# Optimization experiments

Measured on AMD Instinct MI355X. Metric: run time of the kernel, lower is better.

The kernel has to match this reference:

```python
import jax, jax.numpy as jnp
import numpy as np

NQ = 200000; K = 4; M = 64; KEY = 64; V = 128; E = 64; B = 512; S = 200

def setup_inputs() -> dict:
    key = jax.random.key(0)
    ks = jax.random.split(key, 16)
    return {
        'q_embed_table': jax.random.normal(ks[0], (NQ + 1, E), jnp.float32) * 0.1,
        'alpha_mean': jax.random.normal(ks[1], (NQ,), jnp.float32) * 0.2,
        'beta_base': jax.random.normal(ks[2], (NQ,), jnp.float32) * 0.5,
        'beta_gaps': jax.random.uniform(ks[3], (NQ, K - 2), jnp.float32) * 0.5 + 0.25,
        'ability_means': jax.random.normal(ks[4], (M, V), jnp.float32) * 0.1,
        'ability_log_vars': jnp.zeros((M, V), jnp.float32),
        'memory_keys': jax.random.normal(ks[5], (M, KEY), jnp.float32),
        'q_to_key_w': jax.random.normal(ks[6], (E, KEY), jnp.float32) / np.sqrt(E),
        'q_to_key_b': jnp.zeros((KEY,), jnp.float32),
        'qa_embed_w': jax.random.normal(ks[7], (2, E), jnp.float32),
        'qa_embed_b': jnp.zeros((E,), jnp.float32),
        'qa_to_ev_w': jax.random.normal(ks[8], (E, V), jnp.float32) / np.sqrt(E),
        'qa_to_ev_b': jnp.zeros((V,), jnp.float32),
        'questions': jax.random.randint(ks[9], (B, S), 0, NQ),
        'responses': jax.random.randint(ks[10], (B, S), 0, K),
    }


def reference(q_embed_table, alpha_mean, beta_base, beta_gaps, ability_means,
              ability_log_vars, memory_keys, q_to_key_w, q_to_key_b,
              qa_embed_w, qa_embed_b, qa_to_ev_w, qa_to_ev_b,
              questions, responses):
    nQ = alpha_mean.shape[0]
    Kc = beta_gaps.shape[1] + 2  # n_categories

    # --- gather question-specific IRT params (irregular gather) ---
    alphas = jnp.exp(alpha_mean[questions])                      # [B,S]
    base = beta_base[questions]                                  # [B,S]
    gaps = jax.nn.softplus(beta_gaps[questions])                 # [B,S,K-2]
    # cumulative thresholds: beta_0 = base, beta_k = beta_{k-1} + gap_{k-1}
    betas = jnp.cumsum(jnp.concatenate([base[..., None], gaps], axis=-1), axis=-1)  # [B,S,K-1]

    # --- attention over memory slots ---
    q_emb = q_embed_table[questions]                             # [B,S,E]
    queries = q_emb @ q_to_key_w + q_to_key_b                    # [B,S,KEY]
    attn = jax.nn.softmax(jnp.einsum('bsk,mk->bsm', queries, memory_keys), axis=-1)  # [B,S,M]

    # --- evidence embedding from (question, response) ---
    qn = questions.astype(jnp.float32) / nQ
    rn = responses.astype(jnp.float32) / (Kc - 1)
    qa = jnp.stack([qn, rn], axis=-1) @ qa_embed_w + qa_embed_b  # [B,S,E]
    evidence = jnp.tanh(qa) @ qa_to_ev_w + qa_to_ev_b            # [B,S,V]

    # --- sequential memory read + per-slot Bayesian scatter update ---
    def step(carry, inp):
        means, log_vars = carry                                  # [M,V] each
        attn_t, ev_t = inp                                       # [B,M], [B,V]
        theta = jnp.mean(attn_t @ means, axis=-1)                # bayesian_read -> [B]
        # precision-weighted update of every slot (evidence_precision = 1)
        w = jnp.mean(attn_t, axis=0)                             # [M] update weights
        ev_mean = jnp.mean(ev_t, axis=0)                         # [V]
        prior_prec = jnp.exp(-log_vars)
        post_prec = prior_prec + w[:, None]
        post_mean = (prior_prec * means + ev_mean[None, :] * w[:, None]) / post_prec
        # torch updates under no_grad -> stop_gradient
        new_means = jax.lax.stop_gradient(post_mean)
        new_lv = jax.lax.stop_gradient(-jnp.log(post_prec))
        return (new_means, new_lv), theta

    (_, _), thetas = jax.lax.scan(
        step, (ability_means, ability_log_vars),
        (attn.transpose(1, 0, 2), evidence.transpose(1, 0, 2)))
    thetas = thetas.T                                            # [B,S]

    # --- GPCM category probabilities ---
    z = alphas[..., None] * (thetas[..., None] - betas)          # [B,S,K-1]
    cum = jnp.concatenate([jnp.zeros_like(z[..., :1]), jnp.cumsum(z, axis=-1)], axis=-1)  # [B,S,K]
    probs = jax.nn.softmax(cum, axis=-1)
    return probs
```

## Files before the change

### kernel.cpp

```cpp
#include <hip/hip_runtime.h>
#include <math.h>

#define M_SLOTS 64
#define E_DIM   64
#define KEY_DIM 64
#define V_DIM   128
#define K_CAT   4
#define S_LEN   200

typedef __attribute__((ext_vector_type(8)))  short short8;
typedef __attribute__((ext_vector_type(16))) float f32x16;

#define OFF_CT     0
#define OFF_BM     2048
#define OFF_WBAR   2112
#define OFF_BBAR   2176
#define OFF_RM0    2240
#define OFF_P0     2304
#define OFF_WSUM   2368
#define OFF_EMSUM  (OFF_WSUM + S_LEN*M_SLOTS)
#define ZERO_CNT   (S_LEN*M_SLOTS + S_LEN)

__device__ __forceinline__ unsigned pk2rne(float lo, float hi) {
    unsigned ul = __float_as_uint(lo); ul += 0x7fffu + ((ul >> 16) & 1u);
    unsigned uh = __float_as_uint(hi); uh += 0x7fffu + ((uh >> 16) & 1u);
    return __builtin_amdgcn_perm(uh, ul, 0x07060302u);
}
__device__ __forceinline__ unsigned short bf16rne(float f) {
    unsigned u = __float_as_uint(f);
    return (unsigned short)((u + 0x7fffu + ((u >> 16) & 1u)) >> 16);
}
__device__ __forceinline__ short8 as_s8(uint4 u) { return __builtin_bit_cast(short8, u); }

__device__ __forceinline__ void gpcm_store(float th, int q,
                                           const float* __restrict__ alpha_mean,
                                           const float* __restrict__ beta_base,
                                           const float* __restrict__ beta_gaps,
                                           float* __restrict__ out, size_t idx) {
    float a  = __expf(alpha_mean[q]);
    float b0 = beta_base[q];
    float2 g = *reinterpret_cast<const float2*>(&beta_gaps[q * (K_CAT - 2)]);
    float g0 = log1pf(__expf(g.x));
    float g1 = log1pf(__expf(g.y));
    float be1 = b0 + g0;
    float be2 = be1 + g1;
    float z0 = a * (th - b0);
    float z1 = a * (th - be1);
    float z2 = a * (th - be2);
    float c1 = z0, c2 = z0 + z1, c3 = z0 + z1 + z2;
    float cm = fmaxf(fmaxf(0.f, c1), fmaxf(c2, c3));
    float e0 = __expf(0.f - cm), e1 = __expf(c1 - cm), e2 = __expf(c2 - cm), e3 = __expf(c3 - cm);
    float si = __fdividef(1.0f, e0 + e1 + e2 + e3);
    float4 o4 = make_float4(e0 * si, e1 * si, e2 * si, e3 * si);
    *reinterpret_cast<float4*>(&out[idx * K_CAT]) = o4;
}

__device__ __forceinline__ void load_qf(const float* __restrict__ qrow, int h, float4 qf[8]) {
    #pragma unroll
    for (int s = 0; s < 4; ++s) {
        const float4* src = (const float4*)(qrow + s * 16 + h * 8);
        qf[2 * s]     = src[0];
        qf[2 * s + 1] = src[1];
    }
}

__device__ __forceinline__ void mfma_logits(
    const float4 qf[8], const unsigned short* __restrict__ ct,
    const float* __restrict__ bm, int h, int p, f32x16 acc[2])
{
    uint4 af[8];
    #pragma unroll
    for (int mt = 0; mt < 2; ++mt)
        #pragma unroll
        for (int s = 0; s < 4; ++s)
            af[mt * 4 + s] = *(const uint4*)(ct + (p + 32 * mt) * E_DIM + s * 16 + h * 8);
    #pragma unroll
    for (int mt = 0; mt < 2; ++mt)
        #pragma unroll
        for (int g = 0; g < 4; ++g) {
            float4 v = *(const float4*)(bm + 8 * g + 4 * h + 32 * mt);
            acc[mt][4 * g + 0] = v.x; acc[mt][4 * g + 1] = v.y;
            acc[mt][4 * g + 2] = v.z; acc[mt][4 * g + 3] = v.w;
        }
    #pragma unroll
    for (int s = 0; s < 4; ++s) {
        uint4 bf;
        bf.x = pk2rne(qf[2 * s].x,     qf[2 * s].y);
        bf.y = pk2rne(qf[2 * s].z,     qf[2 * s].w);
        bf.z = pk2rne(qf[2 * s + 1].x, qf[2 * s + 1].y);
        bf.w = pk2rne(qf[2 * s + 1].z, qf[2 * s + 1].w);
        short8 bfr = as_s8(bf);
        acc[0] = __builtin_amdgcn_mfma_f32_32x32x16_bf16(as_s8(af[s]),     bfr, acc[0], 0, 0, 0);
        acc[1] = __builtin_amdgcn_mfma_f32_32x32x16_bf16(as_s8(af[4 + s]), bfr, acc[1], 0, 0, 0);
    }
}

__global__ __launch_bounds__(256) void k_pre(
    const float* __restrict__ q2k_w, const float* __restrict__ q2k_b,
    const float* __restrict__ mkeys,
    const float* __restrict__ ev_w, const float* __restrict__ ev_b,
    const float* __restrict__ means, const float* __restrict__ logvars,
    float* __restrict__ ws)
{
    const int tid = threadIdx.x;
    if (blockIdx.x != 0) {
        int i = ((int)blockIdx.x - 1) * 1024 + tid * 4;
        if (i + 4 <= ZERO_CNT) {
            *reinterpret_cast<float4*>(ws + OFF_WSUM + i) = make_float4(0.f, 0.f, 0.f, 0.f);
        } else {
            for (int j = i; j < ZERO_CNT; ++j) ws[OFF_WSUM + j] = 0.f;
        }
        return;
    }
    const int wv = tid >> 6, lane = tid & 63;
    const int h = lane >> 5, p = lane & 31;

    {
        const int m0 = (wv & 1) * 32, e0 = (wv >> 1) * 32;
        f32x16 d;
        #pragma unroll
        for (int i = 0; i < 16; ++i) d[i] = 0.f;
        #pragma unroll
        for (int s = 0; s < 4; ++s) {
            const float* ar = mkeys + (m0 + p) * KEY_DIM + s * 16 + h * 8;
            const float* br = q2k_w + (e0 + p) * KEY_DIM + s * 16 + h * 8;
            float4 a0 = *(const float4*)ar, a1 = *(const float4*)(ar + 4);
            float4 b0 = *(const float4*)br, b1 = *(const float4*)(br + 4);
            uint4 au, bu;
            au.x = pk2rne(a0.x, a0.y); au.y = pk2rne(a0.z, a0.w);
            au.z = pk2rne(a1.x, a1.y); au.w = pk2rne(a1.z, a1.w);
            bu.x = pk2rne(b0.x, b0.y); bu.y = pk2rne(b0.z, b0.w);
            bu.z = pk2rne(b1.x, b1.y); bu.w = pk2rne(b1.z, b1.w);
            d = __builtin_amdgcn_mfma_f32_32x32x16_bf16(as_s8(au), as_s8(bu), d, 0, 0, 0);
        }
        unsigned short* ct = (unsigned short*)ws;
        #pragma unroll
        for (int j = 0; j < 16; ++j) {
            int row = (j & 3) + 8 * ((j >> 2) & 3) + 4 * h;
            ct[(m0 + row) * E_DIM + e0 + p] = bf16rne(d[j]);
        }
    }

    if (wv == 0) {
        float s = 0.f;
        const float4* er = (const float4*)(ev_w + (size_t)lane * V_DIM);
        #pragma unroll
        for (int i = 0; i < V_DIM / 4; ++i) {
            float4 v = er[i];
            s += (v.x + v.y) + (v.z + v.w);
        }
        ws[OFF_WBAR + lane] = s * (1.0f / V_DIM);
    } else if (wv == 1) {
        float s = 0.f;
        const float4* mk = (const float4*)(mkeys + lane * KEY_DIM);
        const float4* qb = (const float4*)q2k_b;
        #pragma unroll
        for (int i = 0; i < KEY_DIM / 4; ++i) {
            float4 a = mk[i], c = qb[i];
            s += a.x * c.x + a.y * c.y + a.z * c.z + a.w * c.w;
        }
        ws[OFF_BM + lane] = s;
        float bbv = ev_b[lane] + ev_b[64 + lane];
        #pragma unroll
        for (int o = 32; o; o >>= 1) bbv += __shfl_xor(bbv, o);
        if (!lane) ws[OFF_BBAR] = bbv * (1.0f / V_DIM);
    } else if (wv == 2) {
        float s = 0.f;
        const float4* mr = (const float4*)(means + (size_t)lane * V_DIM);
        #pragma unroll
        for (int i = 0; i < V_DIM / 4; ++i) {
            float4 v = mr[i];
            s += (v.x + v.y) + (v.z + v.w);
        }
        ws[OFF_RM0 + lane] = s * (1.0f / V_DIM);
        ws[OFF_P0 + lane]  = __expf(-logvars[(size_t)lane * V_DIM]);
    }
}

__global__ __launch_bounds__(256, 4) void k_attn(
    const float* __restrict__ qtab, const int* __restrict__ qs, const int* __restrict__ rs,
    const float* __restrict__ ws_ro,
    const float* __restrict__ qa_w, const float* __restrict__ qa_b,
    float* __restrict__ wsum, float* __restrict__ emsum,
    int B, float invNQ)
{
    __shared__ float4 lsEv[64];
    const int tid = threadIdx.x, wv = tid >> 6, lane = tid & 63;
    const int h = lane >> 5, p = lane & 31;
    const int t = blockIdx.x;
    const int b = blockIdx.y * 128 + wv * 32 + p;

    const int q = qs[(size_t)b * S_LEN + t];
    const int r = rs[(size_t)b * S_LEN + t];
    float4 qf[8];
    load_qf(qtab + (size_t)q * E_DIM, h, qf);

    if (tid < 64) lsEv[tid] = make_float4(qa_w[tid], qa_w[E_DIM + tid], qa_b[tid],
                                          ws_ro[OFF_WBAR + tid]);
    const float bb = ws_ro[OFF_BBAR];

    f32x16 acc[2];
    mfma_logits(qf, (const unsigned short*)ws_ro, ws_ro + OFF_BM, h, p, acc);

    float av[32];
    float ssum = 0.f;
    #pragma unroll
    for (int j = 0; j < 16; ++j) { av[j]      = __expf(acc[0][j]); ssum += av[j]; }
    #pragma unroll
    for (int j = 0; j < 16; ++j) { av[16 + j] = __expf(acc[1][j]); ssum += av[16 + j]; }
    ssum += __shfl_xor(ssum, 32);
    const float inv = __fdividef(1.0f, ssum);

    #pragma unroll
    for (int j = 0; j < 32; ++j) av[j] *= inv;
    #pragma unroll
    for (int step = 0; step < 5; ++step) {
        const int sh = 1 << step;
        #pragma unroll
        for (int j = 0; j < (32 >> step) / 2; ++j) {
            float p0 = av[2 * j]     + __shfl_xor(av[2 * j], sh);
            float p1 = av[2 * j + 1] + __shfl_xor(av[2 * j + 1], sh);
            av[j] = (lane & sh) ? p1 : p0;
        }
    }
    {
        const int jj = lane & 31;
        const int m = (jj & 3) + 8 * ((jj >> 2) & 3) + 4 * h + 32 * (jj >> 4);
        atomicAdd(&wsum[t * M_SLOTS + m], av[0]);
    }

    __syncthreads();

    float qn = (float)q * invNQ;
    float rn = (float)r * (1.0f / (K_CAT - 1));
    float evm = 0.f;
    #pragma unroll 8
    for (int e = 0; e < 32; ++e) {
        float4 pv = lsEv[h * 32 + e];
        float qa = fmaf(qn, pv.x, fmaf(rn, pv.y, pv.z));
        float ez = __expf(2.0f * qa);
        evm = fmaf(__fdividef(ez - 1.0f, ez + 1.0f), pv.w, evm);
    }
    evm += __shfl_xor(evm, 32);
    evm += bb;
    #pragma unroll
    for (int o = 16; o; o >>= 1) evm += __shfl_xor(evm, o);
    if (!lane) atomicAdd(&emsum[t], evm);
}

__global__ __launch_bounds__(256, 4) void k_out(
    const float* __restrict__ qtab, const int* __restrict__ qs,
    const float* __restrict__ ws_ro,
    const float* __restrict__ alpha_mean, const float* __restrict__ beta_base,
    const float* __restrict__ beta_gaps, float* __restrict__ out, int B, float invB)
{
    __shared__ float lsW[4][M_SLOTS], lsN[4][M_SLOTS];
    __shared__ float lsRmP[M_SLOTS];
    const int tid = threadIdx.x, wv = tid >> 6, lane = tid & 63;
    const int h = lane >> 5, p = lane & 31;
    const int t = blockIdx.x;
    const int b = blockIdx.y * 128 + wv * 32 + p;

    const int q = qs[(size_t)b * S_LEN + t];
    float4 qf[8];
    load_qf(qtab + (size_t)q * E_DIM, h, qf);

    {
        const float* wsum  = ws_ro + OFF_WSUM;
        const float* emsum = ws_ro + OFF_EMSUM;
        const int seg = (t + 3) >> 2;
        const int s0 = wv * seg, s1 = min(s0 + seg, t);
        float pw0 = 0.f, pn0 = 0.f, pw1 = 0.f, pn1 = 0.f;
        int s = s0;
        for (; s + 2 <= s1; s += 2) {
            float w0 = wsum[s * M_SLOTS + lane];
            float w1 = wsum[(s + 1) * M_SLOTS + lane];
            float e0 = emsum[s], e1 = emsum[s + 1];
            pw0 += w0; pn0 = fmaf(e0, w0, pn0);
            pw1 += w1; pn1 = fmaf(e1, w1, pn1);
        }
        if (s < s1) {
            float w = wsum[s * M_SLOTS + lane];
            pw0 += w; pn0 = fmaf(emsum[s], w, pn0);
        }
        lsW[wv][lane] = pw0 + pw1; lsN[wv][lane] = pn0 + pn1;
    }
    __syncthreads();
    if (tid < 64) {
        const int m = tid;
        float sw = lsW[0][m] + lsW[1][m] + lsW[2][m] + lsW[3][m];
        float sn = lsN[0][m] + lsN[1][m] + lsN[2][m] + lsN[3][m];
        float den = ws_ro[OFF_P0 + m] + sw * invB;
        float num = fmaf(ws_ro[OFF_P0 + m], ws_ro[OFF_RM0 + m], sn * (invB * invB));
        const int idx = ((m >> 2) & 1) * 32 + ((m >> 5) & 1) * 16 + (m & 3) + 4 * ((m >> 3) & 3);
        lsRmP[idx] = num / den;
    }
    __syncthreads();

    f32x16 acc[2];
    mfma_logits(qf, (const unsigned short*)ws_ro, ws_ro + OFF_BM, h, p, acc);

    float ssum = 0.f, th = 0.f;
    const float* rmh = lsRmP + h * 32;
    #pragma unroll
    for (int j = 0; j < 16; ++j) {
        float e = __expf(acc[0][j]);
        ssum += e;
        th = fmaf(e, rmh[j], th);
    }
    #pragma unroll
    for (int j = 0; j < 16; ++j) {
        float e = __expf(acc[1][j]);
        ssum += e;
        th = fmaf(e, rmh[16 + j], th);
    }
    ssum += __shfl_xor(ssum, 32);
    th   += __shfl_xor(th, 32);
    th = __fdividef(th, ssum);

    if (!h) gpcm_store(th, q, alpha_mean, beta_base, beta_gaps, out, (size_t)b * S_LEN + t);
}

extern "C" void kernel_launch(void* const* d_in, const int* in_sizes, int n_in,
                              void* d_out, int out_size, void* d_ws, size_t ws_size,
                              hipStream_t stream) {
    const float* qtab       = (const float*)d_in[0];
    const float* alpha_mean = (const float*)d_in[1];
    const float* beta_base  = (const float*)d_in[2];
    const float* beta_gaps  = (const float*)d_in[3];
    const float* ab_means   = (const float*)d_in[4];
    const float* ab_logvars = (const float*)d_in[5];
    const float* mkeys      = (const float*)d_in[6];
    const float* q2k_w      = (const float*)d_in[7];
    const float* q2k_b      = (const float*)d_in[8];
    const float* qa_w       = (const float*)d_in[9];
    const float* qa_b       = (const float*)d_in[10];
    const float* ev_w       = (const float*)d_in[11];
    const float* ev_b       = (const float*)d_in[12];
    const int*   qs         = (const int*)d_in[13];
    const int*   rs         = (const int*)d_in[14];
    float* out = (float*)d_out;
    float* ws  = (float*)d_ws;

    const int NQ = in_sizes[1];
    const int S  = S_LEN;
    const int B  = in_sizes[13] / S;

    float* wsum  = ws + OFF_WSUM;
    float* emsum = ws + OFF_EMSUM;

    k_pre<<<14, 256, 0, stream>>>(q2k_w, q2k_b, mkeys, ev_w, ev_b,
                                  ab_means, ab_logvars, ws);

    dim3 g(S, B / 128);
    k_attn<<<g, 256, 0, stream>>>(qtab, qs, rs, ws, qa_w, qa_b,
                                  wsum, emsum, B, 1.0f / (float)NQ);

    k_out<<<g, 256, 0, stream>>>(qtab, qs, ws, alpha_mean, beta_base,
                                 beta_gaps, out, B, 1.0f / (float)B);
}
```

Measured before the change: 47.16 us.

## Process two timesteps per block in attention and output kernels

Each block of k_attn and k_out now handles two consecutive timesteps instead of one, and the grid's time dimension is halved. In k_out the prefix sum over earlier steps is computed once for t0, and the t1 value is derived by adding a single step, which avoids a second pass over the prefix. The change also issues more independent gathers per thread for latency hiding and lowers the launch-bounds occupancy hint from 4 to 3. In exchange it raises register pressure and leaves fewer blocks to spread across CUs.

```diff
diff --git a/kernel.cpp b/kernel.cpp
--- a/kernel.cpp
+++ b/kernel.cpp
@@ -95,6 +95,35 @@
     }
 }
 
+__device__ __forceinline__ void softmax_fold_store(
+    const f32x16 acc[2], int lane, int h, int t,
+    float* __restrict__ wsum)
+{
+    float av[32];
+    float ssum = 0.f;
+    #pragma unroll
+    for (int j = 0; j < 16; ++j) { av[j]      = __expf(acc[0][j]); ssum += av[j]; }
+    #pragma unroll
+    for (int j = 0; j < 16; ++j) { av[16 + j] = __expf(acc[1][j]); ssum += av[16 + j]; }
+    ssum += __shfl_xor(ssum, 32);
+    const float inv = __fdividef(1.0f, ssum);
+    #pragma unroll
+    for (int j = 0; j < 32; ++j) av[j] *= inv;
+    #pragma unroll
+    for (int step = 0; step < 5; ++step) {
+        const int sh = 1 << step;
+        #pragma unroll
+        for (int j = 0; j < (32 >> step) / 2; ++j) {
+            float p0 = av[2 * j]     + __shfl_xor(av[2 * j], sh);
+            float p1 = av[2 * j + 1] + __shfl_xor(av[2 * j + 1], sh);
+            av[j] = (lane & sh) ? p1 : p0;
+        }
+    }
+    const int jj = lane & 31;
+    const int m = (jj & 3) + 8 * ((jj >> 2) & 3) + 4 * h + 32 * (jj >> 4);
+    atomicAdd(&wsum[t * M_SLOTS + m], av[0]);
+}
+
 __global__ __launch_bounds__(256) void k_pre(
     const float* __restrict__ q2k_w, const float* __restrict__ q2k_b,
     const float* __restrict__ mkeys,
@@ -177,7 +206,7 @@
     }
 }
 
-__global__ __launch_bounds__(256, 4) void k_attn(
+__global__ __launch_bounds__(256, 3) void k_attn(
     const float* __restrict__ qtab, const int* __restrict__ qs, const int* __restrict__ rs,
     const float* __restrict__ ws_ro,
     const float* __restrict__ qa_w, const float* __restrict__ qa_b,
@@ -187,89 +216,81 @@
     __shared__ float4 lsEv[64];
     const int tid = threadIdx.x, wv = tid >> 6, lane = tid & 63;
     const int h = lane >> 5, p = lane & 31;
-    const int t = blockIdx.x;
+    const int t0 = blockIdx.x * 2, t1 = t0 + 1;
     const int b = blockIdx.y * 128 + wv * 32 + p;
 
-    const int q = qs[(size_t)b * S_LEN + t];
-    const int r = rs[(size_t)b * S_LEN + t];
-    float4 qf[8];
-    load_qf(qtab + (size_t)q * E_DIM, h, qf);
+    const int q0 = qs[(size_t)b * S_LEN + t0];
+    const int r0 = rs[(size_t)b * S_LEN + t0];
+    const int q1 = qs[(size_t)b * S_LEN + t1];
+    const int r1 = rs[(size_t)b * S_LEN + t1];
+    float4 qf0[8], qf1[8];
+    load_qf(qtab + (size_t)q0 * E_DIM, h, qf0);
+    load_qf(qtab + (size_t)q1 * E_DIM, h, qf1);
 
     if (tid < 64) lsEv[tid] = make_float4(qa_w[tid], qa_w[E_DIM + tid], qa_b[tid],
                                           ws_ro[OFF_WBAR + tid]);
     const float bb = ws_ro[OFF_BBAR];
 
-    f32x16 acc[2];
-    mfma_logits(qf, (const unsigned short*)ws_ro, ws_ro + OFF_BM, h, p, acc);
-
-    float av[32];
-    float ssum = 0.f;
-    #pragma unroll
-    for (int j = 0; j < 16; ++j) { av[j]      = __expf(acc[0][j]); ssum += av[j]; }
-    #pragma unroll
-    for (int j = 0; j < 16; ++j) { av[16 + j] = __expf(acc[1][j]); ssum += av[16 + j]; }
-    ssum += __shfl_xor(ssum, 32);
-    const float inv = __fdividef(1.0f, ssum);
-
-    #pragma unroll
-    for (int j = 0; j < 32; ++j) av[j] *= inv;
-    #pragma unroll
-    for (int step = 0; step < 5; ++step) {
-        const int sh = 1 << step;
-        #pragma unroll
-        for (int j = 0; j < (32 >> step) / 2; ++j) {
-            float p0 = av[2 * j]     + __shfl_xor(av[2 * j], sh);
-            float p1 = av[2 * j + 1] + __shfl_xor(av[2 * j + 1], sh);
-            av[j] = (lane & sh) ? p1 : p0;
-        }
-    }
     {
-        const int jj = lane & 31;
-        const int m = (jj & 3) + 8 * ((jj >> 2) & 3) + 4 * h + 32 * (jj >> 4);
-        atomicAdd(&wsum[t * M_SLOTS + m], av[0]);
+        f32x16 acc[2];
+        mfma_logits(qf0, (const unsigned short*)ws_ro, ws_ro + OFF_BM, h, p, acc);
+        softmax_fold_store(acc, lane, h, t0, wsum);
+    }
+    {
+        f32x16 acc[2];
+        mfma_logits(qf1, (const unsigned short*)ws_ro, ws_ro + OFF_BM, h, p, acc);
+        softmax_fold_store(acc, lane, h, t1, wsum);
     }
 
     __syncthreads();
 
-    float qn = (float)q * invNQ;
-    float rn = (float)r * (1.0f / (K_CAT - 1));
-    float evm = 0.f;
+    float ev0 = 0.f, ev1 = 0.f;
+    const float qn0 = (float)q0 * invNQ, rn0 = (float)r0 * (1.0f / (K_CAT - 1));
+    const float qn1 = (float)q1 * invNQ, rn1 = (float)r1 * (1.0f / (K_CAT - 1));
     #pragma unroll 8
     for (int e = 0; e < 32; ++e) {
         float4 pv = lsEv[h * 32 + e];
-        float qa = fmaf(qn, pv.x, fmaf(rn, pv.y, pv.z));
-        float ez = __expf(2.0f * qa);
-        evm = fmaf(__fdividef(ez - 1.0f, ez + 1.0f), pv.w, evm);
-    }
-    evm += __shfl_xor(evm, 32);
-    evm += bb;
-    #pragma unroll
-    for (int o = 16; o; o >>= 1) evm += __shfl_xor(evm, o);
-    if (!lane) atomicAdd(&emsum[t], evm);
-}
-
-__global__ __launch_bounds__(256, 4) void k_out(
+        float qa0 = fmaf(qn0, pv.x, fmaf(rn0, pv.y, pv.z));
+        float qa1 = fmaf(qn1, pv.x, fmaf(rn1, pv.y, pv.z));
+        float ez0 = __expf(2.0f * qa0);
+        float ez1 = __expf(2.0f * qa1);
+        ev0 = fmaf(__fdividef(ez0 - 1.0f, ez0 + 1.0f), pv.w, ev0);
+        ev1 = fmaf(__fdividef(ez1 - 1.0f, ez1 + 1.0f), pv.w, ev1);
+    }
+    ev0 += __shfl_xor(ev0, 32); ev0 += bb;
+    ev1 += __shfl_xor(ev1, 32); ev1 += bb;
+    #pragma unroll
+    for (int o = 16; o; o >>= 1) { ev0 += __shfl_xor(ev0, o); ev1 += __shfl_xor(ev1, o); }
+    if (!lane) {
+        atomicAdd(&emsum[t0], ev0);
+        atomicAdd(&emsum[t1], ev1);
+    }
+}
+
+__global__ __launch_bounds__(256, 3) void k_out(
     const float* __restrict__ qtab, const int* __restrict__ qs,
     const float* __restrict__ ws_ro,
     const float* __restrict__ alpha_mean, const float* __restrict__ beta_base,
     const float* __restrict__ beta_gaps, float* __restrict__ out, int B, float invB)
 {
     __shared__ float lsW[4][M_SLOTS], lsN[4][M_SLOTS];
-    __shared__ float lsRmP[M_SLOTS];
+    __shared__ float lsRmP0[M_SLOTS], lsRmP1[M_SLOTS];
     const int tid = threadIdx.x, wv = tid >> 6, lane = tid & 63;
     const int h = lane >> 5, p = lane & 31;
-    const int t = blockIdx.x;
+    const int t0 = blockIdx.x * 2, t1 = t0 + 1;
     const int b = blockIdx.y * 128 + wv * 32 + p;
 
-    const int q = qs[(size_t)b * S_LEN + t];
-    float4 qf[8];
-    load_qf(qtab + (size_t)q * E_DIM, h, qf);
+    const int q0 = qs[(size_t)b * S_LEN + t0];
+    const int q1 = qs[(size_t)b * S_LEN + t1];
+    float4 qf0[8], qf1[8];
+    load_qf(qtab + (size_t)q0 * E_DIM, h, qf0);
+    load_qf(qtab + (size_t)q1 * E_DIM, h, qf1);
 
     {
         const float* wsum  = ws_ro + OFF_WSUM;
         const float* emsum = ws_ro + OFF_EMSUM;
-        const int seg = (t + 3) >> 2;
-        const int s0 = wv * seg, s1 = min(s0 + seg, t);
+        const int seg = (t0 + 3) >> 2;
+        const int s0 = wv * seg, s1 = min(s0 + seg, t0);
         float pw0 = 0.f, pn0 = 0.f, pw1 = 0.f, pn1 = 0.f;
         int s = s0;
         for (; s + 2 <= s1; s += 2) {
@@ -290,35 +311,46 @@
         const int m = tid;
         float sw = lsW[0][m] + lsW[1][m] + lsW[2][m] + lsW[3][m];
         float sn = lsN[0][m] + lsN[1][m] + lsN[2][m] + lsN[3][m];
-        float den = ws_ro[OFF_P0 + m] + sw * invB;
-        float num = fmaf(ws_ro[OFF_P0 + m], ws_ro[OFF_RM0 + m], sn * (invB * invB));
+        const float p0v = ws_ro[OFF_P0 + m];
+        float den0 = p0v + sw * invB;
+        float num0 = fmaf(p0v, ws_ro[OFF_RM0 + m], sn * (invB * invB));
+        float wstep = ws_ro[OFF_WSUM + t0 * M_SLOTS + m];
+        float estep = ws_ro[OFF_EMSUM + t0];
+        float den1 = den0 + wstep * invB;
+        float num1 = fmaf(estep * wstep, invB * invB, num0);
         const int idx = ((m >> 2) & 1) * 32 + ((m >> 5) & 1) * 16 + (m & 3) + 4 * ((m >> 3) & 3);
-        lsRmP[idx] = num / den;
+        lsRmP0[idx] = num0 / den0;
+        lsRmP1[idx] = num1 / den1;
     }
     __syncthreads();
 
-    f32x16 acc[2];
-    mfma_logits(qf, (const unsigned short*)ws_ro, ws_ro + OFF_BM, h, p, acc);
-
-    float ssum = 0.f, th = 0.f;
-    const float* rmh = lsRmP + h * 32;
-    #pragma unroll
-    for (int j = 0; j < 16; ++j) {
-        float e = __expf(acc[0][j]);
-        ssum += e;
-        th = fmaf(e, rmh[j], th);
-    }
-    #pragma unroll
-    for (int j = 0; j < 16; ++j) {
-        float e = __expf(acc[1][j]);
-        ssum += e;
-        th = fmaf(e, rmh[16 + j], th);
-    }
-    ssum += __shfl_xor(ssum, 32);
-    th   += __shfl_xor(th, 32);
-    th = __fdividef(th, ssum);
-
-    if (!h) gpcm_store(th, q, alpha_mean, beta_base, beta_gaps, out, (size_t)b * S_LEN + t);
+    #pragma unroll
+    for (int it = 0; it < 2; ++it) {
+        f32x16 acc[2];
+        mfma_logits(it ? qf1 : qf0, (const unsigned short*)ws_ro, ws_ro + OFF_BM, h, p, acc);
+        const float* rmh = (it ? lsRmP1 : lsRmP0) + h * 32;
+        float ssum = 0.f, th = 0.f;
+        #pragma unroll
+        for (int j = 0; j < 16; ++j) {
+            float e = __expf(acc[0][j]);
+            ssum += e;
+            th = fmaf(e, rmh[j], th);
+        }
+        #pragma unroll
+        for (int j = 0; j < 16; ++j) {
+            float e = __expf(acc[1][j]);
+            ssum += e;
+            th = fmaf(e, rmh[16 + j], th);
+        }
+        ssum += __shfl_xor(ssum, 32);
+        th   += __shfl_xor(th, 32);
+        th = __fdividef(th, ssum);
+        if (!h) {
+            const int t = it ? t1 : t0;
+            const int q = it ? q1 : q0;
+            gpcm_store(th, q, alpha_mean, beta_base, beta_gaps, out, (size_t)b * S_LEN + t);
+        }
+    }
 }
 
 extern "C" void kernel_launch(void* const* d_in, const int* in_sizes, int n_in,
@@ -352,7 +384,7 @@
     k_pre<<<14, 256, 0, stream>>>(q2k_w, q2k_b, mkeys, ev_w, ev_b,
                                   ab_means, ab_logvars, ws);
 
-    dim3 g(S, B / 128);
+    dim3 g(S / 2, B / 128);
     k_attn<<<g, 256, 0, stream>>>(qtab, qs, rs, ws, qa_w, qa_b,
                                   wsum, emsum, B, 1.0f / (float)NQ);
 
```

Measured after the change: 45.78 us. 2.9% less time.
